# Performance work log

Hardware: AMD Instinct MI355X
Metric: run time of the kernel (lower is better)

Reference implementation:

```python
import jax, jax.numpy as jnp
import numpy as np

N_EMBD = 1024
N_HEAD = 16
HEAD_DIM = N_EMBD // N_HEAD
BLOCK_SIZE = 2048
ROPE_BASE = 10000.0


def _rope_tables(dim, max_len, base=ROPE_BASE):
    half = dim // 2
    freqs = 1.0 / base ** (jnp.arange(half, dtype=jnp.float32) / half)
    angles = jnp.arange(max_len, dtype=jnp.float32)[:, None] * freqs[None, :]  # (T, half)
    return jnp.cos(angles), jnp.sin(angles)


def _apply_rope(x, cos, sin):
    # x: (B, H, T, D); cos/sin: (T, D//2)
    T = x.shape[2]
    c = cos[:T][None, None]
    s = sin[:T][None, None]
    x1 = x[..., ::2]
    x2 = x[..., 1::2]
    out = jnp.stack([x1 * c - x2 * s, x1 * s + x2 * c], axis=-1)  # (B,H,T,D//2,2)
    return out.reshape(x.shape)


def setup_inputs() -> dict:
    key = jax.random.key(0)
    k1, k2, k3, k4, k5 = jax.random.split(key, 5)
    B, T, C = 2, 2048, N_EMBD
    x = jax.random.normal(k1, (B, T, C), dtype=jnp.float32)
    scale = 1.0 / np.sqrt(C)
    Wqkv = jax.random.normal(k2, (C, 3 * C), dtype=jnp.float32) * scale
    bqkv = jax.random.normal(k3, (3 * C,), dtype=jnp.float32) * 0.01
    Wproj = jax.random.normal(k4, (C, C), dtype=jnp.float32) * scale
    bproj = jax.random.normal(k5, (C,), dtype=jnp.float32) * 0.01
    cos, sin = _rope_tables(HEAD_DIM, BLOCK_SIZE)
    return {"x": x, "Wqkv": Wqkv, "bqkv": bqkv, "Wproj": Wproj, "bproj": bproj,
            "cos": cos, "sin": sin}


def reference(x, Wqkv, bqkv, Wproj, bproj, cos, sin):
    B, T, C = x.shape
    H, D = N_HEAD, HEAD_DIM
    qkv = x @ Wqkv + bqkv  # (B,T,3C)
    q, k, v = jnp.split(qkv, 3, axis=-1)
    # (B,T,C) -> (B,H,T,D)
    q = q.reshape(B, T, H, D).transpose(0, 2, 1, 3)
    k = k.reshape(B, T, H, D).transpose(0, 2, 1, 3)
    v = v.reshape(B, T, H, D).transpose(0, 2, 1, 3)
    q = _apply_rope(q, cos, sin)
    k = _apply_rope(k, cos, sin)
    att = jnp.einsum('bhtd,bhsd->bhts', q, k) * (D ** -0.5)
    causal = jnp.tril(jnp.ones((T, T), dtype=bool))
    att = jnp.where(causal[None, None], att, -jnp.inf)
    att = jax.nn.softmax(att, axis=-1)
    y = jnp.einsum('bhts,bhsd->bhtd', att, v)  # (B,H,T,D)
    y = y.transpose(0, 2, 1, 3).reshape(B, T, C)
    return y @ Wproj + bproj
```

## Files before the change

kernel.cpp:

```cpp
#include <hip/hip_runtime.h>
#include <stdint.h>

typedef short s16x8 __attribute__((ext_vector_type(8)));
typedef float f32x4 __attribute__((ext_vector_type(4)));
typedef unsigned short u16;
typedef unsigned int u32;

__device__ __forceinline__ float bf2f(u16 u) {
  union { u32 i; float f; } v; v.i = ((u32)u) << 16; return v.f;
}
__device__ __forceinline__ u16 f2bf(float f) {
  union { float f; u32 i; } v; v.f = f;
  u32 i = v.i;
  return (u16)((i + 0x7fffu + ((i >> 16) & 1u)) >> 16);
}
__device__ __forceinline__ u16 f2bf_fast(float f) {
  union { float f; u32 i; } v; v.f = f;
  return (u16)((v.i + 0x8000u) >> 16);
}

__device__ __forceinline__ s16x8 load8(const void* p, size_t idx, int isf32) {
  s16x8 r;
  if (isf32) {
    const float* f = (const float*)p + idx;
    f32x4 a = *(const f32x4*)f;
    f32x4 b = *(const f32x4*)(f + 4);
#pragma unroll
    for (int j = 0; j < 4; j++) {
      r[j] = (short)f2bf(a[j]);
      r[4 + j] = (short)f2bf(b[j]);
    }
  } else {
    r = *(const s16x8*)((const u16*)p + idx);
  }
  return r;
}
__device__ __forceinline__ float loadf(const void* p, size_t idx, int isf32) {
  return isf32 ? ((const float*)p)[idx] : bf2f(((const u16*)p)[idx]);
}

__device__ __forceinline__ void cp16(const u16* g, u16* l) {
  __builtin_amdgcn_global_load_lds(
      (const __attribute__((address_space(1))) u32*)g,
      (__attribute__((address_space(3))) u32*)l, 16, 0, 0);
}

__global__ void detect_dtype(const u16* __restrict__ x, int* __restrict__ flags) {
  int cnt = 0;
  for (int i = threadIdx.x; i < 4096; i += 64) {
    int e = (x[i] >> 7) & 0xFF;
    if (e >= 0xF0) cnt++;
  }
  unsigned long long any = __ballot(cnt > 0);
  if (threadIdx.x == 0) {
    flags[0] = (any != 0ull) ? 1 : 0;
    flags[1] = 0;
  }
}

__global__ __launch_bounds__(256) void convert_x(const void* __restrict__ x,
                                                 const int* __restrict__ fp,
                                                 u16* __restrict__ xb) {
  size_t i = ((size_t)blockIdx.x * 256 + threadIdx.x) * 8;
  *(s16x8*)(xb + i) = load8(x, i, *fp);
}

__global__ __launch_bounds__(256) void transposeW2(
    const void* __restrict__ Wqkv, const void* __restrict__ Wproj,
    const int* __restrict__ fp, u16* __restrict__ WqkvT,
    u16* __restrict__ WprojT) {
  __shared__ u32 tile32[32 * 66];
  const int f = *fp;
  const int tid = threadIdx.x;
  const int bx = blockIdx.x;
  const void* W;
  u16* WT;
  int N, nb;
  if (bx < 48) { W = Wqkv; WT = WqkvT; N = 3072; nb = bx * 64; }
  else         { W = Wproj; WT = WprojT; N = 1024; nb = (bx - 48) * 64; }
  const int kb = blockIdx.y * 64;
  {
    int a = tid >> 3, c8 = tid & 7;
    s16x8 r0 = load8(W, (size_t)(kb + 2 * a) * N + nb + c8 * 8, f);
    s16x8 r1 = load8(W, (size_t)(kb + 2 * a + 1) * N + nb + c8 * 8, f);
#pragma unroll
    for (int j = 0; j < 8; j++)
      tile32[a * 66 + c8 * 8 + j] = (u32)(u16)r0[j] | ((u32)(u16)r1[j] << 16);
  }
  __syncthreads();
#pragma unroll
  for (int i = 0; i < 2; i++) {
    int idx = tid + i * 256;
    int n = idx >> 3, c8 = idx & 7;
    s16x8 v;
#pragma unroll
    for (int w = 0; w < 4; w++) {
      u32 pk = tile32[(c8 * 4 + w) * 66 + n];
      v[2 * w] = (short)(u16)(pk & 0xFFFF);
      v[2 * w + 1] = (short)(u16)(pk >> 16);
    }
    *(s16x8*)(WT + (size_t)(nb + n) * 1024 + kb + c8 * 8) = v;
  }
}

__global__ __launch_bounds__(256) void transposeV(const u16* __restrict__ qkv,
                                                  u16* __restrict__ vT) {
  __shared__ u32 tile32[64 * 33];
  const int tid = threadIdx.x;
  const int tb = blockIdx.x * 64, bh = blockIdx.y;
  const int b = bh >> 4, h = bh & 15;
  {
    int a = tid >> 3, c8 = tid & 7;
    const u16* base = qkv + (size_t)(b * 2048 + tb + 2 * a) * 3072 + 2048 + h * 64;
    s16x8 r0 = *(const s16x8*)(base + c8 * 8);
    s16x8 r1 = *(const s16x8*)(base + 3072 + c8 * 8);
#pragma unroll
    for (int j = 0; j < 8; j++)
      tile32[(c8 * 8 + j) * 33 + a] = (u32)(u16)r0[j] | ((u32)(u16)r1[j] << 16);
  }
  __syncthreads();
#pragma unroll
  for (int i = 0; i < 2; i++) {
    int idx = tid + i * 256;
    int d = idx >> 3, c8 = idx & 7;
    s16x8 v;
#pragma unroll
    for (int w = 0; w < 4; w++) {
      u32 pk = tile32[d * 33 + c8 * 4 + w];
      v[2 * w] = (short)(u16)(pk & 0xFFFF);
      v[2 * w + 1] = (short)(u16)(pk >> 16);
    }
    *(s16x8*)(vT + ((size_t)bh * 64 + d) * 2048 + tb + c8 * 8) = v;
  }
}

template <int NT>
__global__ __launch_bounds__(256) void gemm_bt(
    const u16* __restrict__ A, int lda, const u16* __restrict__ Bt,
    const void* __restrict__ bias, const int* __restrict__ fI32,
    void* __restrict__ C, int ropeMode, int outF,
    const void* __restrict__ cost, const void* __restrict__ sint, int N,
    int K) {
  constexpr int NTW = NT / 32;
  __shared__ __attribute__((aligned(16))) u16 As[128 * 32];
  __shared__ __attribute__((aligned(16))) u16 Bs[NT * 32];
  const int inf32 = *fI32;
  const int tid = threadIdx.x;
  const int wave = tid >> 6, lane = tid & 63, quad = lane >> 4, l16 = lane & 15;
  const int m0 = blockIdx.y * 128, n0 = blockIdx.x * NT;
  const int wm = (wave & 1) * 64, wn = (wave >> 1) * (NT / 2);
  const int lr = lane >> 2, lk = (lane & 3) * 8;
  f32x4 acc[4][NTW];
#pragma unroll
  for (int i = 0; i < 4; i++)
#pragma unroll
    for (int j = 0; j < NTW; j++) acc[i][j] = (f32x4){0.f, 0.f, 0.f, 0.f};

  const u16* aP = A + (size_t)(m0 + wave * 32 + lr) * lda + lk;
  const u16* bP = Bt + (size_t)(n0 + wave * (NT / 4) + lr) * K + lk;
  u16* asl = As + wave * 32 * 32;
  u16* bsl = Bs + wave * (NT / 4) * 32;

  for (int kb = 0; kb < K; kb += 32) {
    __syncthreads();
    cp16(aP + kb, asl);
    cp16(aP + kb + (size_t)16 * lda, asl + 16 * 32);
#pragma unroll
    for (int i = 0; i < NT / 64; i++)
      cp16(bP + kb + (size_t)(16 * i) * K, bsl + i * 16 * 32);
    __syncthreads();
    s16x8 af[4], bfr[NTW];
#pragma unroll
    for (int t = 0; t < 4; t++)
      af[t] = *(const s16x8*)(As + (wm + t * 16 + l16) * 32 + quad * 8);
#pragma unroll
    for (int t = 0; t < NTW; t++)
      bfr[t] = *(const s16x8*)(Bs + (wn + t * 16 + l16) * 32 + quad * 8);
#pragma unroll
    for (int mt = 0; mt < 4; mt++)
#pragma unroll
      for (int nt = 0; nt < NTW; nt++)
        acc[mt][nt] = __builtin_amdgcn_mfma_f32_16x16x32_bf16(
            af[mt], bfr[nt], acc[mt][nt], 0, 0, 0);
  }
#pragma unroll
  for (int nt = 0; nt < NTW; nt++) {
    int col = n0 + wn + nt * 16 + l16;
    float bv = loadf(bias, col, inf32);
    if (ropeMode && col < 2048) {
      int j = (col & 63) >> 1, odd = col & 1;
#pragma unroll
      for (int mt = 0; mt < 4; mt++)
#pragma unroll
        for (int r = 0; r < 4; r++) {
          int row = m0 + wm + mt * 16 + quad * 4 + r, t = row & 2047;
          float cv = loadf(cost, (size_t)t * 32 + j, inf32);
          float sv = loadf(sint, (size_t)t * 32 + j, inf32);
          float val = acc[mt][nt][r] + bv;
          float pr = __shfl_xor(val, 1);
          float res = odd ? (pr * sv + val * cv) : (val * cv - pr * sv);
          ((u16*)C)[(size_t)row * N + col] = f2bf(res);
        }
    } else if (outF && inf32) {
#pragma unroll
      for (int mt = 0; mt < 4; mt++)
#pragma unroll
        for (int r = 0; r < 4; r++) {
          int row = m0 + wm + mt * 16 + quad * 4 + r;
          ((float*)C)[(size_t)row * N + col] = acc[mt][nt][r] + bv;
        }
    } else {
#pragma unroll
      for (int mt = 0; mt < 4; mt++)
#pragma unroll
        for (int r = 0; r < 4; r++) {
          int row = m0 + wm + mt * 16 + quad * 4 + r;
          ((u16*)C)[(size_t)row * N + col] = f2bf(acc[mt][nt][r] + bv);
        }
    }
  }
}

__global__ __launch_bounds__(512) void attn_kernel(u16* qkv,
                                                   const u16* __restrict__ vT) {
  __shared__ __attribute__((aligned(16))) u16 Ks[64 * 72];
  __shared__ __attribute__((aligned(16))) u16 Vt[64 * 72];
  __shared__ __attribute__((aligned(16))) u16 Pl[8][16 * 72];
  const int tid = threadIdx.x;
  const int wave = tid >> 6, lane = tid & 63, quad = lane >> 4, l16 = lane & 15;
  const int cu = blockIdx.x & 255, round = blockIdx.x >> 8;
  const int p = cu >> 5, bh = cu & 31;
  const int qt = round ? p : 15 - p;
  const int h = bh & 15;
  const size_t rb = (size_t)(bh >> 4) * 2048;
  const int qb = qt * 128;
  const float SCALE = 0.18033688011112042f;

  s16x8 qa0, qa1;
  {
    const u16* qp = qkv + (rb + qb + wave * 16 + l16) * 3072 + h * 64;
    qa0 = *(const s16x8*)(qp + quad * 8);
    qa1 = *(const s16x8*)(qp + 32 + quad * 8);
  }

  f32x4 o[4];
  float l_r[4] = {0.f, 0.f, 0.f, 0.f};
#pragma unroll
  for (int i = 0; i < 4; i++) o[i] = (f32x4){0.f, 0.f, 0.f, 0.f};

  const int nchunks = 2 * qt + 2;
  const int srow = tid >> 3, sc8 = tid & 7;
  s16x8 kr, vr;
  {
    kr = *(const s16x8*)(qkv + (rb + srow) * 3072 + 1024 + h * 64 + sc8 * 8);
    vr = *(const s16x8*)(vT + ((size_t)bh * 64 + srow) * 2048 + sc8 * 8);
  }

  for (int c = 0; c < nchunks; c++) {
    const int sb = c * 64;
    __syncthreads();
    *(s16x8*)(Ks + srow * 72 + sc8 * 8) = kr;
    *(s16x8*)(Vt + srow * 72 + sc8 * 8) = vr;
    __syncthreads();
    if (c + 1 < nchunks) {
      const int nb = sb + 64;
      kr = *(const s16x8*)(qkv + (rb + nb + srow) * 3072 + 1024 + h * 64 +
                           sc8 * 8);
      vr = *(const s16x8*)(vT + ((size_t)bh * 64 + srow) * 2048 + nb + sc8 * 8);
    }

    if (sb > qb + wave * 16 + 15) continue;

    f32x4 S[4];
#pragma unroll
    for (int kf = 0; kf < 4; kf++) {
      s16x8 k0 = *(const s16x8*)(Ks + (kf * 16 + l16) * 72 + quad * 8);
      s16x8 k1 = *(const s16x8*)(Ks + (kf * 16 + l16) * 72 + 32 + quad * 8);
      f32x4 a = (f32x4){0.f, 0.f, 0.f, 0.f};
      a = __builtin_amdgcn_mfma_f32_16x16x32_bf16(qa0, k0, a, 0, 0, 0);
      a = __builtin_amdgcn_mfma_f32_16x16x32_bf16(qa1, k1, a, 0, 0, 0);
      S[kf] = a;
    }

    u16* P = Pl[wave];
    const int mq = qb + wave * 16;
    const bool needMask = (sb + 63) > mq;
#pragma unroll
    for (int r = 0; r < 4; r++) {
      const int qi = mq + quad * 4 + r;
#pragma unroll
      for (int kf = 0; kf < 4; kf++) {
        float pv = __builtin_amdgcn_exp2f(S[kf][r] * SCALE);
        if (needMask) pv = ((sb + kf * 16 + l16) <= qi) ? pv : 0.f;
        l_r[r] += pv;
        P[(quad * 4 + r) * 72 + kf * 16 + l16] = f2bf_fast(pv);
      }
    }
    asm volatile("s_waitcnt lgkmcnt(0)" ::: "memory");
    s16x8 pa0 = *(const s16x8*)(P + l16 * 72 + quad * 8);
    s16x8 pa1 = *(const s16x8*)(P + l16 * 72 + 32 + quad * 8);

#pragma unroll
    for (int dt = 0; dt < 4; dt++) {
      s16x8 vb0 = *(const s16x8*)(Vt + (dt * 16 + l16) * 72 + quad * 8);
      s16x8 vb1 = *(const s16x8*)(Vt + (dt * 16 + l16) * 72 + 32 + quad * 8);
      o[dt] = __builtin_amdgcn_mfma_f32_16x16x32_bf16(pa0, vb0, o[dt], 0, 0, 0);
      o[dt] = __builtin_amdgcn_mfma_f32_16x16x32_bf16(pa1, vb1, o[dt], 0, 0, 0);
    }
  }

  float inv[4];
#pragma unroll
  for (int r = 0; r < 4; r++) {
    float rs = l_r[r];
#pragma unroll
    for (int off = 8; off; off >>= 1) rs += __shfl_xor(rs, off);
    inv[r] = 1.0f / fmaxf(rs, 1e-30f);
  }
#pragma unroll
  for (int dt = 0; dt < 4; dt++)
#pragma unroll
    for (int r = 0; r < 4; r++)
      qkv[(rb + qb + wave * 16 + quad * 4 + r) * 3072 + 2048 + h * 64 +
          dt * 16 + l16] = f2bf(o[dt][r] * inv[r]);
}

extern "C" void kernel_launch(void* const* d_in, const int* in_sizes, int n_in,
                              void* d_out, int out_size, void* d_ws,
                              size_t ws_size, hipStream_t stream) {
  const void* x = d_in[0];
  const void* Wqkv = d_in[1];
  const void* bqkv = d_in[2];
  const void* Wproj = d_in[3];
  const void* bproj = d_in[4];
  const void* cost = d_in[5];
  const void* sint = d_in[6];

  int* flags = (int*)d_ws;
  u16* WqkvT = (u16*)d_ws + 128;
  u16* WprojT = WqkvT + (size_t)3072 * 1024;
  u16* qkv = WprojT + (size_t)1024 * 1024;
  u16* yb = qkv + 2048;
  u16* xb = (u16*)d_out;
  u16* vT = (u16*)d_out + (size_t)4096 * 1024;

  detect_dtype<<<1, 64, 0, stream>>>((const u16*)x, flags);
  convert_x<<<2048, 256, 0, stream>>>(x, flags, xb);
  transposeW2<<<dim3(64, 16), 256, 0, stream>>>(Wqkv, Wproj, flags, WqkvT,
                                                WprojT);
  gemm_bt<128><<<dim3(24, 32), 256, 0, stream>>>(
      xb, 1024, WqkvT, bqkv, flags, qkv, 1, 0, cost, sint, 3072, 1024);
  transposeV<<<dim3(32, 32), 256, 0, stream>>>(qkv, vT);
  attn_kernel<<<512, 512, 0, stream>>>(qkv, vT);
  gemm_bt<64><<<dim3(16, 32), 256, 0, stream>>>(
      yb, 3072, WprojT, bproj, flags, d_out, 0, 1, nullptr, nullptr, 1024,
      1024);
}
```

Baseline: 212.4 us.

## Triple-buffer GEMM LDS tiles with async prefetch and raise MFMA priority in attention

```diff
diff --git a/kernel.cpp b/kernel.cpp
--- a/kernel.cpp
+++ b/kernel.cpp
@@ -134,16 +134,16 @@
   }
 }
 
-template <int NT>
+template <int NT, int KK>
 __global__ __launch_bounds__(256) void gemm_bt(
     const u16* __restrict__ A, int lda, const u16* __restrict__ Bt,
     const void* __restrict__ bias, const int* __restrict__ fI32,
     void* __restrict__ C, int ropeMode, int outF,
-    const void* __restrict__ cost, const void* __restrict__ sint, int N,
-    int K) {
+    const void* __restrict__ cost, const void* __restrict__ sint, int N) {
   constexpr int NTW = NT / 32;
-  __shared__ __attribute__((aligned(16))) u16 As[128 * 32];
-  __shared__ __attribute__((aligned(16))) u16 Bs[NT * 32];
+  constexpr int NTILES = KK / 32;
+  __shared__ __attribute__((aligned(16))) u16 As[3][128 * 32];
+  __shared__ __attribute__((aligned(16))) u16 Bs[3][NT * 32];
   const int inf32 = *fI32;
   const int tid = threadIdx.x;
   const int wave = tid >> 6, lane = tid & 63, quad = lane >> 4, l16 = lane & 15;
@@ -157,32 +157,61 @@
     for (int j = 0; j < NTW; j++) acc[i][j] = (f32x4){0.f, 0.f, 0.f, 0.f};
 
   const u16* aP = A + (size_t)(m0 + wave * 32 + lr) * lda + lk;
-  const u16* bP = Bt + (size_t)(n0 + wave * (NT / 4) + lr) * K + lk;
-  u16* asl = As + wave * 32 * 32;
-  u16* bsl = Bs + wave * (NT / 4) * 32;
-
-  for (int kb = 0; kb < K; kb += 32) {
-    __syncthreads();
-    cp16(aP + kb, asl);
-    cp16(aP + kb + (size_t)16 * lda, asl + 16 * 32);
+  const u16* bP = Bt + (size_t)(n0 + wave * (NT / 4) + lr) * KK + lk;
+  const int aWo = wave * 32 * 32;
+  const int bWo = wave * (NT / 4) * 32;
+
+  u16 *aCur = &As[0][0], *aNxt = &As[1][0], *aStg = &As[2][0];
+  u16 *bCur = &Bs[0][0], *bNxt = &Bs[1][0], *bStg = &Bs[2][0];
+
+  auto STAGE = [&](int tt, u16* ad0, u16* bd0) {
+    const int kb = tt * 32;
+    u16* ad = ad0 + aWo;
+    u16* bd = bd0 + bWo;
+    cp16(aP + kb, ad);
+    cp16(aP + kb + (size_t)16 * lda, ad + 16 * 32);
 #pragma unroll
     for (int i = 0; i < NT / 64; i++)
-      cp16(bP + kb + (size_t)(16 * i) * K, bsl + i * 16 * 32);
-    __syncthreads();
+      cp16(bP + kb + (size_t)(16 * i) * KK, bd + i * 16 * 32);
+  };
+
+  STAGE(0, aCur, bCur);
+  STAGE(1, aNxt, bNxt);
+
+  for (int t = 0; t < NTILES; ++t) {
+    __builtin_amdgcn_s_barrier();
+    if (t + 2 < NTILES) {
+      STAGE(t + 2, aStg, bStg);
+      if constexpr (NT == 128) asm volatile("s_waitcnt vmcnt(8)" ::: "memory");
+      else                     asm volatile("s_waitcnt vmcnt(6)" ::: "memory");
+    } else if (t + 1 < NTILES) {
+      if constexpr (NT == 128) asm volatile("s_waitcnt vmcnt(4)" ::: "memory");
+      else                     asm volatile("s_waitcnt vmcnt(3)" ::: "memory");
+    } else {
+      asm volatile("s_waitcnt vmcnt(0)" ::: "memory");
+    }
+    __builtin_amdgcn_s_barrier();
+    asm volatile("" ::: "memory");
+
     s16x8 af[4], bfr[NTW];
 #pragma unroll
-    for (int t = 0; t < 4; t++)
-      af[t] = *(const s16x8*)(As + (wm + t * 16 + l16) * 32 + quad * 8);
-#pragma unroll
-    for (int t = 0; t < NTW; t++)
-      bfr[t] = *(const s16x8*)(Bs + (wn + t * 16 + l16) * 32 + quad * 8);
+    for (int tt = 0; tt < 4; tt++)
+      af[tt] = *(const s16x8*)(aCur + (wm + tt * 16 + l16) * 32 + quad * 8);
+#pragma unroll
+    for (int tt = 0; tt < NTW; tt++)
+      bfr[tt] = *(const s16x8*)(bCur + (wn + tt * 16 + l16) * 32 + quad * 8);
 #pragma unroll
     for (int mt = 0; mt < 4; mt++)
 #pragma unroll
       for (int nt = 0; nt < NTW; nt++)
         acc[mt][nt] = __builtin_amdgcn_mfma_f32_16x16x32_bf16(
             af[mt], bfr[nt], acc[mt][nt], 0, 0, 0);
-  }
+
+    u16* ta = aCur; aCur = aNxt; aNxt = aStg; aStg = ta;
+    u16* tb = bCur; bCur = bNxt; bNxt = bStg; bStg = tb;
+    asm volatile("" ::: "memory");
+  }
+
 #pragma unroll
   for (int nt = 0; nt < NTW; nt++) {
     int col = n0 + wn + nt * 16 + l16;
@@ -272,6 +301,7 @@
     if (sb > qb + wave * 16 + 15) continue;
 
     f32x4 S[4];
+    __builtin_amdgcn_s_setprio(1);
 #pragma unroll
     for (int kf = 0; kf < 4; kf++) {
       s16x8 k0 = *(const s16x8*)(Ks + (kf * 16 + l16) * 72 + quad * 8);
@@ -281,6 +311,7 @@
       a = __builtin_amdgcn_mfma_f32_16x16x32_bf16(qa1, k1, a, 0, 0, 0);
       S[kf] = a;
     }
+    __builtin_amdgcn_s_setprio(0);
 
     u16* P = Pl[wave];
     const int mq = qb + wave * 16;
@@ -300,6 +331,7 @@
     s16x8 pa0 = *(const s16x8*)(P + l16 * 72 + quad * 8);
     s16x8 pa1 = *(const s16x8*)(P + l16 * 72 + 32 + quad * 8);
 
+    __builtin_amdgcn_s_setprio(1);
 #pragma unroll
     for (int dt = 0; dt < 4; dt++) {
       s16x8 vb0 = *(const s16x8*)(Vt + (dt * 16 + l16) * 72 + quad * 8);
@@ -307,6 +339,7 @@
       o[dt] = __builtin_amdgcn_mfma_f32_16x16x32_bf16(pa0, vb0, o[dt], 0, 0, 0);
       o[dt] = __builtin_amdgcn_mfma_f32_16x16x32_bf16(pa1, vb1, o[dt], 0, 0, 0);
     }
+    __builtin_amdgcn_s_setprio(0);
   }
 
   float inv[4];
@@ -348,11 +381,10 @@
   convert_x<<<2048, 256, 0, stream>>>(x, flags, xb);
   transposeW2<<<dim3(64, 16), 256, 0, stream>>>(Wqkv, Wproj, flags, WqkvT,
                                                 WprojT);
-  gemm_bt<128><<<dim3(24, 32), 256, 0, stream>>>(
-      xb, 1024, WqkvT, bqkv, flags, qkv, 1, 0, cost, sint, 3072, 1024);
+  gemm_bt<128, 1024><<<dim3(24, 32), 256, 0, stream>>>(
+      xb, 1024, WqkvT, bqkv, flags, qkv, 1, 0, cost, sint, 3072);
   transposeV<<<dim3(32, 32), 256, 0, stream>>>(qkv, vT);
   attn_kernel<<<512, 512, 0, stream>>>(qkv, vT);
-  gemm_bt<64><<<dim3(16, 32), 256, 0, stream>>>(
-      yb, 3072, WprojT, bproj, flags, d_out, 0, 1, nullptr, nullptr, 1024,
-      1024);
-}
+  gemm_bt<64, 1024><<<dim3(16, 32), 256, 0, stream>>>(
+      yb, 3072, WprojT, bproj, flags, d_out, 0, 1, nullptr, nullptr, 1024);
+}
```

New measurement: 218.0 us. 2.7% more time.

## Pre-tile GEMM operands into contiguous k-block panels for coalesced loads

Applied to the files above, without the earlier changes.

```diff
diff --git a/kernel.cpp b/kernel.cpp
--- a/kernel.cpp
+++ b/kernel.cpp
@@ -61,8 +61,10 @@
 __global__ __launch_bounds__(256) void convert_x(const void* __restrict__ x,
                                                  const int* __restrict__ fp,
                                                  u16* __restrict__ xb) {
-  size_t i = ((size_t)blockIdx.x * 256 + threadIdx.x) * 8;
-  *(s16x8*)(xb + i) = load8(x, i, *fp);
+  int tid = blockIdx.x * 256 + threadIdx.x;
+  int r = tid & 127, kq = (tid >> 7) & 3, kB = (tid >> 9) & 31, mB = tid >> 14;
+  size_t src = (size_t)(mB * 128 + r) * 1024 + kB * 32 + kq * 8;
+  *(s16x8*)(xb + (size_t)tid * 8) = load8(x, src, *fp);
 }
 
 __global__ __launch_bounds__(256) void transposeW2(
@@ -75,9 +77,9 @@
   const int bx = blockIdx.x;
   const void* W;
   u16* WT;
-  int N, nb;
-  if (bx < 48) { W = Wqkv; WT = WqkvT; N = 3072; nb = bx * 64; }
-  else         { W = Wproj; WT = WprojT; N = 1024; nb = (bx - 48) * 64; }
+  int N, nb, qkvSide;
+  if (bx < 48) { W = Wqkv; WT = WqkvT; N = 3072; nb = bx * 64; qkvSide = 1; }
+  else         { W = Wproj; WT = WprojT; N = 1024; nb = (bx - 48) * 64; qkvSide = 0; }
   const int kb = blockIdx.y * 64;
   {
     int a = tid >> 3, c8 = tid & 7;
@@ -91,7 +93,7 @@
 #pragma unroll
   for (int i = 0; i < 2; i++) {
     int idx = tid + i * 256;
-    int n = idx >> 3, c8 = idx & 7;
+    int n = idx & 63, c8 = idx >> 6;
     s16x8 v;
 #pragma unroll
     for (int w = 0; w < 4; w++) {
@@ -99,7 +101,17 @@
       v[2 * w] = (short)(u16)(pk & 0xFFFF);
       v[2 * w + 1] = (short)(u16)(pk >> 16);
     }
-    *(s16x8*)(WT + (size_t)(nb + n) * 1024 + kb + c8 * 8) = v;
+    int R = nb + n, k = kb + c8 * 8;
+    int kB = k >> 5, kq = (k >> 3) & 3;
+    size_t off;
+    if (qkvSide) {
+      int nB = R >> 7, r = R & 127;
+      off = ((size_t)(nB * 32 + kB) * 4 + kq) * 1024 + r * 8;
+    } else {
+      int nB = R >> 6, r = R & 63;
+      off = (size_t)(nB * 32 + kB) * 2048 + kq * 512 + r * 8;
+    }
+    *(s16x8*)(WT + off) = v;
   }
 }
 
@@ -134,14 +146,15 @@
   }
 }
 
-template <int NT>
+template <int NT, int KK, int ATILED>
 __global__ __launch_bounds__(256) void gemm_bt(
     const u16* __restrict__ A, int lda, const u16* __restrict__ Bt,
     const void* __restrict__ bias, const int* __restrict__ fI32,
     void* __restrict__ C, int ropeMode, int outF,
-    const void* __restrict__ cost, const void* __restrict__ sint, int N,
-    int K) {
+    const void* __restrict__ cost, const void* __restrict__ sint, int N) {
   constexpr int NTW = NT / 32;
+  constexpr int KT = KK / 32;
+  constexpr int TB = NT * 32;
   __shared__ __attribute__((aligned(16))) u16 As[128 * 32];
   __shared__ __attribute__((aligned(16))) u16 Bs[NT * 32];
   const int inf32 = *fI32;
@@ -149,33 +162,49 @@
   const int wave = tid >> 6, lane = tid & 63, quad = lane >> 4, l16 = lane & 15;
   const int m0 = blockIdx.y * 128, n0 = blockIdx.x * NT;
   const int wm = (wave & 1) * 64, wn = (wave >> 1) * (NT / 2);
-  const int lr = lane >> 2, lk = (lane & 3) * 8;
   f32x4 acc[4][NTW];
 #pragma unroll
   for (int i = 0; i < 4; i++)
 #pragma unroll
     for (int j = 0; j < NTW; j++) acc[i][j] = (f32x4){0.f, 0.f, 0.f, 0.f};
 
-  const u16* aP = A + (size_t)(m0 + wave * 32 + lr) * lda + lk;
-  const u16* bP = Bt + (size_t)(n0 + wave * (NT / 4) + lr) * K + lk;
-  u16* asl = As + wave * 32 * 32;
-  u16* bsl = Bs + wave * (NT / 4) * 32;
-
-  for (int kb = 0; kb < K; kb += 32) {
+  const u16* aT = nullptr;
+  const u16* aP = nullptr;
+  if constexpr (ATILED) {
+    aT = A + (size_t)blockIdx.y * KT * 4096 + wave * 1024 + lane * 8;
+  } else {
+    const int lr = lane >> 2, lk = (lane & 3) * 8;
+    aP = A + (size_t)(m0 + wave * 32 + lr) * lda + lk;
+  }
+  const u16* bT = Bt + (size_t)blockIdx.x * KT * TB + wave * (NT / 64) * 512 +
+                  lane * 8;
+
+  for (int kB = 0; kB < KT; ++kB) {
     __syncthreads();
-    cp16(aP + kb, asl);
-    cp16(aP + kb + (size_t)16 * lda, asl + 16 * 32);
+    if constexpr (ATILED) {
+      cp16(aT + (size_t)kB * 4096, As + wave * 1024);
+      cp16(aT + (size_t)kB * 4096 + 512, As + wave * 1024 + 512);
+    } else {
+      const int kb = kB * 32;
+      cp16(aP + kb, As + wave * 32 * 32);
+      cp16(aP + kb + (size_t)16 * lda, As + wave * 32 * 32 + 16 * 32);
+    }
 #pragma unroll
     for (int i = 0; i < NT / 64; i++)
-      cp16(bP + kb + (size_t)(16 * i) * K, bsl + i * 16 * 32);
+      cp16(bT + (size_t)kB * TB + i * 512,
+           Bs + (wave * (NT / 64) + i) * 512);
     __syncthreads();
     s16x8 af[4], bfr[NTW];
 #pragma unroll
-    for (int t = 0; t < 4; t++)
-      af[t] = *(const s16x8*)(As + (wm + t * 16 + l16) * 32 + quad * 8);
-#pragma unroll
-    for (int t = 0; t < NTW; t++)
-      bfr[t] = *(const s16x8*)(Bs + (wn + t * 16 + l16) * 32 + quad * 8);
+    for (int tt = 0; tt < 4; tt++) {
+      if constexpr (ATILED)
+        af[tt] = *(const s16x8*)(As + quad * 1024 + (wm + tt * 16 + l16) * 8);
+      else
+        af[tt] = *(const s16x8*)(As + (wm + tt * 16 + l16) * 32 + quad * 8);
+    }
+#pragma unroll
+    for (int tt = 0; tt < NTW; tt++)
+      bfr[tt] = *(const s16x8*)(Bs + quad * (NT * 8) + (wn + tt * 16 + l16) * 8);
 #pragma unroll
     for (int mt = 0; mt < 4; mt++)
 #pragma unroll
@@ -183,6 +212,7 @@
         acc[mt][nt] = __builtin_amdgcn_mfma_f32_16x16x32_bf16(
             af[mt], bfr[nt], acc[mt][nt], 0, 0, 0);
   }
+
 #pragma unroll
   for (int nt = 0; nt < NTW; nt++) {
     int col = n0 + wn + nt * 16 + l16;
@@ -348,11 +378,10 @@
   convert_x<<<2048, 256, 0, stream>>>(x, flags, xb);
   transposeW2<<<dim3(64, 16), 256, 0, stream>>>(Wqkv, Wproj, flags, WqkvT,
                                                 WprojT);
-  gemm_bt<128><<<dim3(24, 32), 256, 0, stream>>>(
-      xb, 1024, WqkvT, bqkv, flags, qkv, 1, 0, cost, sint, 3072, 1024);
+  gemm_bt<128, 1024, 1><<<dim3(24, 32), 256, 0, stream>>>(
+      xb, 1024, WqkvT, bqkv, flags, qkv, 1, 0, cost, sint, 3072);
   transposeV<<<dim3(32, 32), 256, 0, stream>>>(qkv, vT);
   attn_kernel<<<512, 512, 0, stream>>>(qkv, vT);
-  gemm_bt<64><<<dim3(16, 32), 256, 0, stream>>>(
-      yb, 3072, WprojT, bproj, flags, d_out, 0, 1, nullptr, nullptr, 1024,
-      1024);
-}
+  gemm_bt<64, 1024, 0><<<dim3(16, 32), 256, 0, stream>>>(
+      yb, 3072, WprojT, bproj, flags, d_out, 0, 1, nullptr, nullptr, 1024);
+}
```

Result: slower. 218.3 us (+2.8%).
